# Optimization experiments

Measured on AMD Instinct MI355X. Metric: run time of the kernel, lower is better.

The kernel has to match this reference:

```python
import jax, jax.numpy as jnp
import numpy as np

N_HEADS = 16
HEAD_SIZE = 128  # n_embd // n_vq_heads = 2048 // 16
N_OPTIONS = 512


def setup_inputs() -> dict:
    key = jax.random.key(0)
    k1, k2, k3 = jax.random.split(key, 3)
    B, S, E = 4, 2048, N_HEADS * HEAD_SIZE
    x = jax.random.normal(k1, (B, S, E), dtype=jnp.float32)
    vq_head_weights = jax.random.normal(k2, (N_HEADS, N_OPTIONS, HEAD_SIZE), dtype=jnp.float32)
    vq_codebooks = jax.random.normal(k3, (N_HEADS, N_OPTIONS, HEAD_SIZE), dtype=jnp.float32)
    temperature = jnp.float32(1.0)
    return {
        "x": x,
        "vq_head_weights": vq_head_weights,
        "vq_codebooks": vq_codebooks,
        "temperature": temperature,
    }


def reference(x, vq_head_weights, vq_codebooks, temperature):
    # Training-mode forward of VQizer (softmax path).
    B, S, E = x.shape
    H, O, A = vq_head_weights.shape  # heads, options, head_size
    x_prepped = x.reshape(B, S, H, A)
    # per-head logits over codebook options
    logits = jnp.einsum('bsha,hoa->bsho', x_prepped, vq_head_weights)
    probs = jax.nn.softmax(logits / temperature, axis=-1)
    out = jnp.einsum('bsho,hoa->bsha', probs, vq_codebooks)
    return out.reshape(B, S, H * A)
```

## Files before the change

### kernel.cpp

```cpp
#include <hip/hip_runtime.h>
#include <math.h>

#define NHEADS 16
#define HS     128
#define NOPT   512
#define TB     128
#define OC     32
#define NCH    16
#define NITER  16
#define EMB    2048
#define LOG2E  1.44269504088896340736f
#define THRD   11.0f

typedef short bf16x8 __attribute__((ext_vector_type(8)));
typedef _Float16 f16x8 __attribute__((ext_vector_type(8)));
typedef unsigned short u16x8 __attribute__((ext_vector_type(8)));
typedef float f32x4 __attribute__((ext_vector_type(4)));
typedef float f32x16 __attribute__((ext_vector_type(16)));
typedef unsigned u32x4 __attribute__((ext_vector_type(4)));

__device__ __forceinline__ unsigned short f2bf(float f) {
    union { float f; unsigned u; } v; v.f = f;
    unsigned r = v.u + 0x7FFFu + ((v.u >> 16) & 1u);
    return (unsigned short)(r >> 16);
}
__device__ __forceinline__ float bf2f(unsigned short h) {
    union { unsigned u; float f; } v; v.u = ((unsigned)h) << 16;
    return v.f;
}
__device__ __forceinline__ unsigned short f2h(float f) {
    const _Float16 h = (_Float16)f;
    return __builtin_bit_cast(unsigned short, h);
}
__device__ __forceinline__ void gll16(const void* gptr, void* lptr) {
    __builtin_amdgcn_global_load_lds(
        (const __attribute__((address_space(1))) void*)gptr,
        (__attribute__((address_space(3))) void*)lptr,
        16, 0, 0);
}
__device__ __forceinline__ unsigned pkrtz(float lo, float hi) {
    unsigned r;
    asm("v_cvt_pkrtz_f16_f32 %0, %1, %2" : "=v"(r) : "v"(lo), "v"(hi));
    return r;
}
__device__ __forceinline__ void pl32swap(unsigned &a, unsigned &b) {
    asm volatile("v_permlane32_swap_b32 %0, %1" : "+v"(a), "+v"(b));
}
__device__ __forceinline__ f32x16 mfma32h(f16x8 a, f16x8 b, f32x16 c) {
    return __builtin_amdgcn_mfma_f32_32x32x16_f16(a, b, c, 0, 0, 0);
}

#define SUBELEMS 4096
#define WS_C0  (NHEADS * NCH * SUBELEMS)
#define WS_TOTAL_BYTES ((size_t)(WS_C0 + NHEADS * NCH * SUBELEMS) * 2)

__global__ __launch_bounds__(256) void vq_prep(const float* __restrict__ W,
                                               const float* __restrict__ C,
                                               const float* __restrict__ temp,
                                               unsigned short* __restrict__ ws)
{
    const int b = blockIdx.x, t = threadIdx.x;
    if (b < NHEADS * NCH) {
        const float scW = (1.0f / temp[0]) * LOG2E;
        const float* src = W + (size_t)b * OC * HS;
        unsigned short* dst = ws + (size_t)b * SUBELEMS;
        #pragma unroll
        for (int i = 0; i < 2; ++i) {
            const int pid = i * 256 + t;
            const int kb = pid >> 6, l = pid & 63;
            const int base = (l & 31) * 128 + kb * 16 + (l >> 5) * 8;
            const float4 v0 = *(const float4*)(src + base);
            const float4 v1 = *(const float4*)(src + base + 4);
            u16x8 hh;
            hh[0] = f2h(v0.x * scW); hh[1] = f2h(v0.y * scW);
            hh[2] = f2h(v0.z * scW); hh[3] = f2h(v0.w * scW);
            hh[4] = f2h(v1.x * scW); hh[5] = f2h(v1.y * scW);
            hh[6] = f2h(v1.z * scW); hh[7] = f2h(v1.w * scW);
            *(u16x8*)&dst[kb * 512 + l * 8] = hh;
        }
    } else {
        const int b2 = b - NHEADS * NCH;
        const float* src = C + (size_t)b2 * OC * HS;
        unsigned short* dst = ws + WS_C0 + (size_t)b2 * SUBELEMS;
        #pragma unroll
        for (int i = 0; i < 2; ++i) {
            const int pid = i * 256 + t;
            const int ntq = pid >> 6, l = pid & 63;
            const int nt = ntq >> 1, q = ntq & 1;
            const int a = nt * 32 + (l & 31);
            const int o0 = q * 16 + (l >> 5) * 8;
            u16x8 hh;
            #pragma unroll
            for (int j = 0; j < 8; ++j) hh[j] = f2h(src[(o0 + j) * 128 + a]);
            *(u16x8*)&dst[ntq * 512 + l * 8] = hh;
        }
    }
}

__global__ __launch_bounds__(256, 2) void vq_main(
    const float* __restrict__ x, const unsigned short* __restrict__ ws,
    float* __restrict__ out)
{
    __shared__ unsigned short wbuf[2][SUBELEMS];
    __shared__ unsigned short cbuf[2][SUBELEMS];

    const int t = threadIdx.x, l = t & 63, w = t >> 6;
    const int la = l & 31, hf = l >> 5;
    const int b = blockIdx.x;
    const int head = ((b & 7) << 1) | ((b >> 3) & 1);
    const int n0 = (b >> 4) * TB;

    const char* gwbase = (const char*)(ws + (size_t)(head * NCH) * SUBELEMS);
    const char* gcbase = (const char*)(ws + WS_C0 + (size_t)(head * NCH) * SUBELEMS);
    const int l8 = l * 8;

    {
        const char* gw = gwbase + w * 2048 + l * 16;
        char* lw = (char*)&wbuf[0][0] + w * 2048;
        const char* gc = gcbase + w * 2048 + l * 16;
        char* lc = (char*)&cbuf[0][0] + w * 2048;
        gll16(gw, lw); gll16(gw + 1024, lw + 1024);
        gll16(gc, lc); gll16(gc + 1024, lc + 1024);
    }

    f16x8 xf[8];
    {
        const float* xr = x + (size_t)(n0 + w * 32 + la) * EMB + head * HS + hf * 8;
        #pragma unroll
        for (int kb = 0; kb < 8; ++kb) {
            const float4 v0 = *(const float4*)(xr + kb * 16);
            const float4 v1 = *(const float4*)(xr + kb * 16 + 4);
            const float vv[8] = {v0.x, v0.y, v0.z, v0.w, v1.x, v1.y, v1.z, v1.w};
            u16x8 hh;
            #pragma unroll
            for (int j = 0; j < 8; ++j) hh[j] = f2h(vv[j]);
            xf[kb] = __builtin_bit_cast(f16x8, hh);
        }
    }

    f32x16 O0 = (f32x16)0.0f, O1 = (f32x16)0.0f, O2 = (f32x16)0.0f, O3 = (f32x16)0.0f;
    float M = -1.0e30f, sacc = 0.0f;

    asm volatile("s_waitcnt vmcnt(0)" ::: "memory");
    __builtin_amdgcn_s_barrier();

    for (int cc = 0; cc < NITER; ++cc) {
        const int cur = cc & 1;
        if (cc + 1 < NITER) {
            const char* gw = gwbase + (size_t)(cc + 1) * 8192 + w * 2048 + l * 16;
            char* lw = (char*)&wbuf[cur ^ 1][0] + w * 2048;
            const char* gc = gcbase + (size_t)(cc + 1) * 8192 + w * 2048 + l * 16;
            char* lc = (char*)&cbuf[cur ^ 1][0] + w * 2048;
            gll16(gw, lw); gll16(gw + 1024, lw + 1024);
            gll16(gc, lc); gll16(gc + 1024, lc + 1024);
        }

        f32x16 S = (f32x16)0.0f;
        const unsigned short* wb = &wbuf[cur][0];
        __builtin_amdgcn_s_setprio(1);
        #pragma unroll
        for (int kb = 0; kb < 8; ++kb)
            S = mfma32h(*(const f16x8*)&wb[kb * 512 + l8], xf[kb], S);
        __builtin_amdgcn_s_setprio(0);

        float cmax = fmaxf(S[0], S[1]);
        #pragma unroll
        for (int i = 2; i < 16; i += 2) cmax = fmaxf(fmaxf(cmax, S[i]), S[i + 1]);
        cmax = fmaxf(cmax, __shfl_xor(cmax, 32));
        if (__any(cmax > M + THRD)) {
            const float Mn = fmaxf(M, cmax);
            const float fr = exp2f(M - Mn);
            M = Mn;
            sacc *= fr;
            #pragma unroll
            for (int q = 0; q < 16; ++q) {
                const int row = (q & 3) + 8 * (q >> 2) + 4 * hf;
                const float f = __shfl(fr, row);
                O0[q] *= f; O1[q] *= f; O2[q] *= f; O3[q] *= f;
            }
        }
        #pragma unroll
        for (int q = 0; q < 16; ++q) S[q] = exp2f(S[q] - M);
        {
            float s8[8];
            #pragma unroll
            for (int i = 0; i < 8; ++i) s8[i] = S[2 * i] + S[2 * i + 1];
            sacc += ((s8[0] + s8[1]) + (s8[2] + s8[3])) +
                    ((s8[4] + s8[5]) + (s8[6] + s8[7]));
        }

        unsigned pk0 = pkrtz(S[0],  S[1]),  pk1 = pkrtz(S[2],  S[3]);
        unsigned pk2 = pkrtz(S[4],  S[5]),  pk3 = pkrtz(S[6],  S[7]);
        unsigned pk4 = pkrtz(S[8],  S[9]),  pk5 = pkrtz(S[10], S[11]);
        unsigned pk6 = pkrtz(S[12], S[13]), pk7 = pkrtz(S[14], S[15]);
        pl32swap(pk0, pk2); pl32swap(pk1, pk3);
        pl32swap(pk4, pk6); pl32swap(pk5, pk7);
        const f16x8 pa0 = __builtin_bit_cast(f16x8, (u32x4){pk0, pk1, pk2, pk3});
        const f16x8 pa1 = __builtin_bit_cast(f16x8, (u32x4){pk4, pk5, pk6, pk7});

        const unsigned short* cb = &cbuf[cur][0];
        __builtin_amdgcn_s_setprio(1);
        #pragma unroll
        for (int nt = 0; nt < 4; ++nt) {
            f32x16& O = (nt == 0) ? O0 : (nt == 1) ? O1 : (nt == 2) ? O2 : O3;
            O = mfma32h(pa0, *(const f16x8*)&cb[(nt * 2 + 0) * 512 + l8], O);
            O = mfma32h(pa1, *(const f16x8*)&cb[(nt * 2 + 1) * 512 + l8], O);
        }
        __builtin_amdgcn_s_setprio(0);

        asm volatile("s_waitcnt vmcnt(0)" ::: "memory");
        if (cc + 1 < NITER) __builtin_amdgcn_s_barrier();
    }

    const float stot = sacc + __shfl_xor(sacc, 32);
    const float rs = 1.0f / stot;
    #pragma unroll
    for (int q = 0; q < 16; ++q) {
        const int row = (q & 3) + 8 * (q >> 2) + 4 * hf;
        const float rq = __shfl(rs, row);
        float* op = out + (size_t)(n0 + w * 32 + row) * EMB + head * HS + la;
        op[0]  = O0[q] * rq;
        op[32] = O1[q] * rq;
        op[64] = O2[q] * rq;
        op[96] = O3[q] * rq;
    }
}

__global__ __launch_bounds__(256, 2) void vq_fwd_mfma(
    const float* __restrict__ x, const float* __restrict__ W,
    const float* __restrict__ C, const float* __restrict__ temp,
    float* __restrict__ out)
{
    __shared__ unsigned short xh_lds[64 * HS];
    __shared__ unsigned short xl_lds[64 * HS];
    __shared__ unsigned short wst[2][64 * HS];
    __shared__ unsigned short p_lds[4][16 * 64];

    const int t = threadIdx.x, l = t & 63, w = t >> 6, lr = l & 15, lk = l >> 4;
    const int b = blockIdx.x;
    const int h = ((b & 7) << 1) | ((b >> 3) & 1);
    const int n0 = (b >> 4) * 64;
    const float invT = 1.0f / temp[0];

    #pragma unroll
    for (int kk = 0; kk < 4; ++kk) {
        const int g = t + 256 * kk;
        const int row = g >> 4, c8 = (g & 15) * 8;
        const float* src = x + (size_t)(n0 + row) * EMB + h * HS + c8;
        const float4 v0 = *(const float4*)src;
        const float4 v1 = *(const float4*)(src + 4);
        float vv[8] = {v0.x, v0.y, v0.z, v0.w, v1.x, v1.y, v1.z, v1.w};
        u16x8 hh, ll;
        #pragma unroll
        for (int j = 0; j < 8; ++j) {
            const unsigned short hb = f2bf(vv[j]);
            hh[j] = hb; ll[j] = f2bf(vv[j] - bf2f(hb));
        }
        const int idx = row * HS + (c8 ^ ((row & 7) << 3));
        *(u16x8*)&xh_lds[idx] = hh;
        *(u16x8*)&xl_lds[idx] = ll;
    }

    f32x4 acc[32];
    #pragma unroll
    for (int i = 0; i < 32; ++i) acc[i] = f32x4{0.f, 0.f, 0.f, 0.f};
    bf16x8 axh[4], axl[4];

    #pragma unroll
    for (int c = 0; c < 8; ++c) {
        if (c) __syncthreads();
        #pragma unroll
        for (int kk = 0; kk < 4; ++kk) {
            const int g = t + 256 * kk;
            const int row = g >> 4, c8 = (g & 15) * 8;
            const float* src = W + ((size_t)h * NOPT + c * 64 + row) * HS + c8;
            const float4 v0 = *(const float4*)src;
            const float4 v1 = *(const float4*)(src + 4);
            float vv[8] = {v0.x, v0.y, v0.z, v0.w, v1.x, v1.y, v1.z, v1.w};
            u16x8 hh, ll;
            #pragma unroll
            for (int j = 0; j < 8; ++j) {
                const unsigned short hb = f2bf(vv[j]);
                hh[j] = hb; ll[j] = f2bf(vv[j] - bf2f(hb));
            }
            const int idx = row * HS + (c8 ^ ((row & 7) << 3));
            *(u16x8*)&wst[0][idx] = hh;
            *(u16x8*)&wst[1][idx] = ll;
        }
        __syncthreads();
        if (c == 0) {
            const int arow = w * 16 + lr;
            #pragma unroll
            for (int ks = 0; ks < 4; ++ks) {
                const int ai = arow * HS + ((lk * 8 + ks * 32) ^ ((arow & 7) << 3));
                axh[ks] = *(const bf16x8*)&xh_lds[ai];
                axl[ks] = *(const bf16x8*)&xl_lds[ai];
            }
        }
        #pragma unroll
        for (int nt = 0; nt < 4; ++nt) {
            const int brow = nt * 16 + lr;
            #pragma unroll
            for (int ks = 0; ks < 4; ++ks) {
                const int bi = brow * HS + ((lk * 8 + ks * 32) ^ ((brow & 7) << 3));
                const bf16x8 bh = *(const bf16x8*)&wst[0][bi];
                const bf16x8 bl = *(const bf16x8*)&wst[1][bi];
                acc[c*4+nt] = __builtin_amdgcn_mfma_f32_16x16x32_bf16(axh[ks], bh, acc[c*4+nt], 0, 0, 0);
                acc[c*4+nt] = __builtin_amdgcn_mfma_f32_16x16x32_bf16(axl[ks], bh, acc[c*4+nt], 0, 0, 0);
                acc[c*4+nt] = __builtin_amdgcn_mfma_f32_16x16x32_bf16(axh[ks], bl, acc[c*4+nt], 0, 0, 0);
            }
        }
    }

    float mx[4], rsn[4];
    #pragma unroll
    for (int r = 0; r < 4; ++r) {
        float m = -3.0e38f;
        #pragma unroll
        for (int i = 0; i < 32; ++i) m = fmaxf(m, acc[i][r]);
        m *= invT;
        #pragma unroll
        for (int s = 1; s < 16; s <<= 1) m = fmaxf(m, __shfl_xor(m, s));
        float sum = 0.f;
        #pragma unroll
        for (int i = 0; i < 32; ++i) sum += exp2f((acc[i][r] * invT - m) * LOG2E);
        #pragma unroll
        for (int s = 1; s < 16; s <<= 1) sum += __shfl_xor(sum, s);
        mx[r] = m; rsn[r] = 1.0f / sum;
    }

    f32x4 oacc[8];
    #pragma unroll
    for (int i = 0; i < 8; ++i) oacc[i] = f32x4{0.f, 0.f, 0.f, 0.f};
    const int pr_ = t & 31, ag = t >> 5;
    #pragma unroll
    for (int c = 0; c < 8; ++c) {
        __syncthreads();
        {
            const float* c0p = C + ((size_t)h * NOPT + c * 64 + 2 * pr_) * HS + ag * 16;
            float va[16], vb[16];
            #pragma unroll
            for (int q = 0; q < 4; ++q) {
                const float4 u0 = ((const float4*)c0p)[q];
                const float4 u1 = ((const float4*)(c0p + HS))[q];
                va[q*4+0] = u0.x; va[q*4+1] = u0.y; va[q*4+2] = u0.z; va[q*4+3] = u0.w;
                vb[q*4+0] = u1.x; vb[q*4+1] = u1.y; vb[q*4+2] = u1.z; vb[q*4+3] = u1.w;
            }
            unsigned* ct32 = (unsigned*)&wst[0][0];
            #pragma unroll
            for (int j = 0; j < 16; ++j) {
                const int a = ag * 16 + j;
                const unsigned pkv = (unsigned)f2bf(va[j]) | ((unsigned)f2bf(vb[j]) << 16);
                ct32[a * 32 + (pr_ ^ ((a & 7) << 2))] = pkv;
            }
        }
        #pragma unroll
        for (int nt = 0; nt < 4; ++nt) {
            #pragma unroll
            for (int r = 0; r < 4; ++r) {
                const float p = exp2f((acc[c*4+nt][r] * invT - mx[r]) * LOG2E);
                const int prow = lk * 4 + r;
                const int pcol = nt * 16 + lr;
                p_lds[w][prow * 64 + (pcol ^ ((prow & 7) << 3))] = f2bf(p);
            }
        }
        __syncthreads();
        #pragma unroll
        for (int ks = 0; ks < 2; ++ks) {
            const int ai = lr * 64 + ((lk * 8 + ks * 32) ^ ((lr & 7) << 3));
            const bf16x8 pa = *(const bf16x8*)&p_lds[w][ai];
            #pragma unroll
            for (int nt = 0; nt < 8; ++nt) {
                const int brow = nt * 16 + lr;
                const int bi = brow * 64 + ((lk * 8 + ks * 32) ^ ((brow & 7) << 3));
                const bf16x8 cbv = *(const bf16x8*)&wst[0][bi];
                oacc[nt] = __builtin_amdgcn_mfma_f32_16x16x32_bf16(pa, cbv, oacc[nt], 0, 0, 0);
            }
        }
    }

    #pragma unroll
    for (int nt = 0; nt < 8; ++nt) {
        #pragma unroll
        for (int r = 0; r < 4; ++r) {
            const int tok = n0 + w * 16 + lk * 4 + r;
            out[(size_t)tok * EMB + h * HS + nt * 16 + lr] = oacc[nt][r] * rsn[r];
        }
    }
}

extern "C" void kernel_launch(void* const* d_in, const int* in_sizes, int n_in,
                              void* d_out, int out_size, void* d_ws, size_t ws_size,
                              hipStream_t stream) {
    const float* x = (const float*)d_in[0];
    const float* W = (const float*)d_in[1];
    const float* C = (const float*)d_in[2];
    const float* T = (const float*)d_in[3];
    float* out     = (float*)d_out;

    const int ntok = in_sizes[0] / EMB;

    if (ws_size >= WS_TOTAL_BYTES) {
        hipLaunchKernelGGL(vq_prep, dim3(NHEADS * NCH * 2), dim3(256), 0, stream,
                           W, C, T, (unsigned short*)d_ws);
        const int nblk = (ntok / TB) * NHEADS;
        hipLaunchKernelGGL(vq_main, dim3(nblk), dim3(256), 0, stream,
                           x, (const unsigned short*)d_ws, out);
    } else {
        const int nblk = (ntok / 64) * NHEADS;
        hipLaunchKernelGGL(vq_fwd_mfma, dim3(nblk), dim3(256), 0, stream,
                           x, W, C, T, out);
    }
}
```

Before: 71.48 us.

## Halve row tile and split output columns across wave pairs for occupancy

The row tile per block drops from 128 to 64. Pairs of waves now share the same 32 rows: each pair recomputes the logits and softmax for those rows, and each wave in the pair produces half of the 128 output columns. This halves the accumulator registers, allowing launch bounds of 4 blocks per CU and doubling the grid. The cost is that the QK^T MFMAs and the exp work are duplicated across each wave pair, and codebook/weight reloads per output row double. The LDS load split is also rearranged so that two waves load W and two load C.

```diff
diff --git a/kernel.cpp b/kernel.cpp
--- a/kernel.cpp
+++ b/kernel.cpp
@@ -4,7 +4,7 @@
 #define NHEADS 16
 #define HS     128
 #define NOPT   512
-#define TB     128
+#define TB     64
 #define OC     32
 #define NCH    16
 #define NITER  16
@@ -97,7 +97,7 @@
     }
 }
 
-__global__ __launch_bounds__(256, 2) void vq_main(
+__global__ __launch_bounds__(256, 4) void vq_main(
     const float* __restrict__ x, const unsigned short* __restrict__ ws,
     float* __restrict__ out)
 {
@@ -106,6 +106,8 @@
 
     const int t = threadIdx.x, l = t & 63, w = t >> 6;
     const int la = l & 31, hf = l >> 5;
+    const int g  = w >> 1;
+    const int hv = w & 1;
     const int b = blockIdx.x;
     const int head = ((b & 7) << 1) | ((b >> 3) & 1);
     const int n0 = (b >> 4) * TB;
@@ -115,17 +117,17 @@
     const int l8 = l * 8;
 
     {
-        const char* gw = gwbase + w * 2048 + l * 16;
-        char* lw = (char*)&wbuf[0][0] + w * 2048;
-        const char* gc = gcbase + w * 2048 + l * 16;
-        char* lc = (char*)&cbuf[0][0] + w * 2048;
-        gll16(gw, lw); gll16(gw + 1024, lw + 1024);
-        gll16(gc, lc); gll16(gc + 1024, lc + 1024);
+        const char* gsrc = (w < 2 ? gwbase + w * 4096
+                                  : gcbase + (w - 2) * 4096) + l * 16;
+        char* ldst = (w < 2 ? (char*)&wbuf[0][0] + w * 4096
+                            : (char*)&cbuf[0][0] + (w - 2) * 4096);
+        #pragma unroll
+        for (int i = 0; i < 4; ++i) gll16(gsrc + i * 1024, ldst + i * 1024);
     }
 
     f16x8 xf[8];
     {
-        const float* xr = x + (size_t)(n0 + w * 32 + la) * EMB + head * HS + hf * 8;
+        const float* xr = x + (size_t)(n0 + g * 32 + la) * EMB + head * HS + hf * 8;
         #pragma unroll
         for (int kb = 0; kb < 8; ++kb) {
             const float4 v0 = *(const float4*)(xr + kb * 16);
@@ -138,7 +140,7 @@
         }
     }
 
-    f32x16 O0 = (f32x16)0.0f, O1 = (f32x16)0.0f, O2 = (f32x16)0.0f, O3 = (f32x16)0.0f;
+    f32x16 O0 = (f32x16)0.0f, O1 = (f32x16)0.0f;
     float M = -1.0e30f, sacc = 0.0f;
 
     asm volatile("s_waitcnt vmcnt(0)" ::: "memory");
@@ -147,12 +149,12 @@
     for (int cc = 0; cc < NITER; ++cc) {
         const int cur = cc & 1;
         if (cc + 1 < NITER) {
-            const char* gw = gwbase + (size_t)(cc + 1) * 8192 + w * 2048 + l * 16;
-            char* lw = (char*)&wbuf[cur ^ 1][0] + w * 2048;
-            const char* gc = gcbase + (size_t)(cc + 1) * 8192 + w * 2048 + l * 16;
-            char* lc = (char*)&cbuf[cur ^ 1][0] + w * 2048;
-            gll16(gw, lw); gll16(gw + 1024, lw + 1024);
-            gll16(gc, lc); gll16(gc + 1024, lc + 1024);
+            const char* gsrc = (w < 2 ? gwbase + (size_t)(cc + 1) * 8192 + w * 4096
+                                      : gcbase + (size_t)(cc + 1) * 8192 + (w - 2) * 4096) + l * 16;
+            char* ldst = (w < 2 ? (char*)&wbuf[cur ^ 1][0] + w * 4096
+                                : (char*)&cbuf[cur ^ 1][0] + (w - 2) * 4096);
+            #pragma unroll
+            for (int i = 0; i < 4; ++i) gll16(gsrc + i * 1024, ldst + i * 1024);
         }
 
         f32x16 S = (f32x16)0.0f;
@@ -176,7 +178,7 @@
             for (int q = 0; q < 16; ++q) {
                 const int row = (q & 3) + 8 * (q >> 2) + 4 * hf;
                 const float f = __shfl(fr, row);
-                O0[q] *= f; O1[q] *= f; O2[q] *= f; O3[q] *= f;
+                O0[q] *= f; O1[q] *= f;
             }
         }
         #pragma unroll
@@ -200,12 +202,10 @@
 
         const unsigned short* cb = &cbuf[cur][0];
         __builtin_amdgcn_s_setprio(1);
-        #pragma unroll
-        for (int nt = 0; nt < 4; ++nt) {
-            f32x16& O = (nt == 0) ? O0 : (nt == 1) ? O1 : (nt == 2) ? O2 : O3;
-            O = mfma32h(pa0, *(const f16x8*)&cb[(nt * 2 + 0) * 512 + l8], O);
-            O = mfma32h(pa1, *(const f16x8*)&cb[(nt * 2 + 1) * 512 + l8], O);
-        }
+        O0 = mfma32h(pa0, *(const f16x8*)&cb[((2 * hv + 0) * 2 + 0) * 512 + l8], O0);
+        O0 = mfma32h(pa1, *(const f16x8*)&cb[((2 * hv + 0) * 2 + 1) * 512 + l8], O0);
+        O1 = mfma32h(pa0, *(const f16x8*)&cb[((2 * hv + 1) * 2 + 0) * 512 + l8], O1);
+        O1 = mfma32h(pa1, *(const f16x8*)&cb[((2 * hv + 1) * 2 + 1) * 512 + l8], O1);
         __builtin_amdgcn_s_setprio(0);
 
         asm volatile("s_waitcnt vmcnt(0)" ::: "memory");
@@ -218,11 +218,9 @@
     for (int q = 0; q < 16; ++q) {
         const int row = (q & 3) + 8 * (q >> 2) + 4 * hf;
         const float rq = __shfl(rs, row);
-        float* op = out + (size_t)(n0 + w * 32 + row) * EMB + head * HS + la;
+        float* op = out + (size_t)(n0 + g * 32 + row) * EMB + head * HS + hv * 64 + la;
         op[0]  = O0[q] * rq;
         op[32] = O1[q] * rq;
-        op[64] = O2[q] * rq;
-        op[96] = O3[q] * rq;
     }
 }
 
```

After: 98.64 us. 38.0% more time.
